# Optimization experiments

Hardware: AMD Instinct MI355X
Metric: run time of the kernel (lower is better)

## Reference

```python
import jax, jax.numpy as jnp
import numpy as np


def setup_inputs() -> dict:
    key = jax.random.key(0)
    ks = jax.random.split(key, 8)
    B, L, C = 8, 4096, 1024
    H = C // 2
    return {
        "x": jax.random.normal(ks[0], (B, L, C), dtype=jnp.float32),
        "w1": jax.random.normal(ks[1], (C, 1), dtype=jnp.float32) * 0.02,
        "b1": jnp.zeros((1,), dtype=jnp.float32),
        "w2": jax.random.normal(ks[2], (C, H), dtype=jnp.float32) * 0.02,
        "b2": jnp.zeros((H,), dtype=jnp.float32),
        "w3": jax.random.normal(ks[3], (H, C), dtype=jnp.float32) * 0.02,
        "b3": jnp.zeros((C,), dtype=jnp.float32),
        "w4": jax.random.normal(ks[4], (C, H), dtype=jnp.float32) * 0.02,
        "b4": jnp.zeros((H,), dtype=jnp.float32),
        "w5": jax.random.normal(ks[5], (C, H), dtype=jnp.float32) * 0.02,
        "b5": jnp.zeros((H,), dtype=jnp.float32),
    }


def reference(x, w1, b1, w2, b2, w3, b3, w4, b4, w5, b5):
    # Polarized self-attention (keras): channel branch then spatial branch.
    B, L, C = x.shape
    # --- channel branch ---
    t1 = x @ w1 + b1                                   # conv1: [B, L, 1]
    t2 = x @ w2 + b2                                   # conv2: [B, L, C/2]
    a = jax.nn.softmax(t1.reshape(B, 1, L), axis=-1)   # reshape1 + softmax: [B, 1, L]
    t2 = jnp.einsum('bol,blh->boh', a, t2)             # dot1 (axes 2,1): [B, 1, C/2]
    t2 = jax.nn.sigmoid(t2 @ w3 + b3)                  # conv3 + sigmoid: [B, 1, C]
    # attention1([inputs, t2]): dot scores [B, L, 1]; softmax over key axis of
    # size 1 is exactly 1.0, so output is t2 broadcast across L (exact math).
    o = jnp.broadcast_to(t2, (B, L, C))                # [B, L, C]
    # --- spatial branch ---
    t1 = o @ w4 + b4                                   # conv4: [B, L, C/2]
    t2 = o @ w5 + b5                                   # conv5: [B, L, C/2]
    t1 = jnp.max(t1, axis=1)[:, :, None]               # global max pool + reshape2: [B, C/2, 1]
    s = jax.nn.sigmoid(jnp.einsum('bho,blh->bol', t1, t2))  # dot2 (axes 1,2) + sigmoid: [B, 1, L]
    # attention2([reshape(o, [B,C,L]), s]): scores [B, C, 1]; softmax over the
    # size-1 key axis is 1.0, so output is s broadcast to [B, C, L] (exact).
    out = jnp.broadcast_to(s, (B, C, L)).reshape(B, L, C)  # reshape4
    return out
```

## Files before the change

### kernel.cpp

```cpp
#include <hip/hip_runtime.h>
#include <stdint.h>

#define B 8
#define L 4096
#define C 1024
#define H 512
#define CCH 64

__global__ __launch_bounds__(256) void k1_t1(const float* __restrict__ x,
                                             const float* __restrict__ w1,
                                             const float* __restrict__ b1,
                                             float* __restrict__ t1) {
    int wave = (blockIdx.x << 2) | ((int)threadIdx.x >> 6);
    int lane = threadIdx.x & 63;
    if (wave >= B * L) return;
    const float4* px = (const float4*)(x + (size_t)wave * C);
    const float4* pw = (const float4*)w1;
    float acc = 0.f;
#pragma unroll
    for (int k = 0; k < 4; ++k) {
        float4 xv = px[lane + 64 * k];
        float4 wv = pw[lane + 64 * k];
        acc += xv.x * wv.x + xv.y * wv.y + xv.z * wv.z + xv.w * wv.w;
    }
#pragma unroll
    for (int off = 32; off > 0; off >>= 1) acc += __shfl_down(acc, off, 64);
    if (lane == 0) t1[wave] = acc + b1[0];
}

__global__ __launch_bounds__(256) void k2_stats(const float* __restrict__ t1,
                                                float* __restrict__ stats,
                                                float* __restrict__ xa,
                                                float* __restrict__ pooled,
                                                float* __restrict__ vraw,
                                                float* __restrict__ u4raw,
                                                float* __restrict__ u5raw) {
    __shared__ float red[256];
    int b = blockIdx.x, t = threadIdx.x;
    const float* tb = t1 + b * L;
    float m = -1e30f;
    for (int i = t; i < L; i += 256) m = fmaxf(m, tb[i]);
    red[t] = m; __syncthreads();
    for (int s = 128; s > 0; s >>= 1) { if (t < s) red[t] = fmaxf(red[t], red[t + s]); __syncthreads(); }
    float mb = red[0]; __syncthreads();
    float sum = 0.f;
    for (int i = t; i < L; i += 256) sum += __expf(tb[i] - mb);
    red[t] = sum; __syncthreads();
    for (int s = 128; s > 0; s >>= 1) { if (t < s) red[t] += red[t + s]; __syncthreads(); }
    if (t == 0) { stats[b * 2] = mb; stats[b * 2 + 1] = 1.f / red[0]; }
    for (int i = t; i < C; i += 256) { xa[b * C + i] = 0.f; vraw[b * C + i] = 0.f; }
    for (int i = t; i < H; i += 256) { pooled[b * H + i] = 0.f; u4raw[b * H + i] = 0.f; u5raw[b * H + i] = 0.f; }
}

__global__ __launch_bounds__(256) void k3_xa(const float* __restrict__ x,
                                             const float* __restrict__ t1,
                                             const float* __restrict__ stats,
                                             float* __restrict__ xa) {
    int b = blockIdx.x >> 6;
    int chunk = blockIdx.x & 63;
    int t = threadIdx.x;
    float mb = stats[b * 2], inv = stats[b * 2 + 1];
    int l0 = chunk * 64;
    float a0 = 0.f, a1 = 0.f, a2 = 0.f, a3 = 0.f;
    for (int i = 0; i < 64; ++i) {
        int l = l0 + i;
        float w = __expf(t1[b * L + l] - mb) * inv;
        float4 xv = *((const float4*)(x + ((size_t)(b * L + l)) * C) + t);
        a0 += w * xv.x;
        a1 += w * xv.y;
        a2 += w * xv.z;
        a3 += w * xv.w;
    }
    int c = t * 4;
    atomicAdd(&xa[b * C + c + 0], a0);
    atomicAdd(&xa[b * C + c + 1], a1);
    atomicAdd(&xa[b * C + c + 2], a2);
    atomicAdd(&xa[b * C + c + 3], a3);
}

__global__ __launch_bounds__(256) void k4a_pooled(const float* __restrict__ xa,
                                                  const float* __restrict__ w2,
                                                  const float* __restrict__ b2,
                                                  float* __restrict__ pooled) {
    __shared__ float xs[B][CCH];
    int hg = blockIdx.x & 1;
    int cc = blockIdx.x >> 1;
    int t = threadIdx.x;
    int c0 = cc * CCH;
    for (int i = t; i < B * CCH; i += 256) {
        int bb = i / CCH, ci = i % CCH;
        xs[bb][ci] = xa[bb * C + c0 + ci];
    }
    __syncthreads();
    int h = hg * 256 + t;
    float acc[B] = {0.f, 0.f, 0.f, 0.f, 0.f, 0.f, 0.f, 0.f};
#pragma unroll 4
    for (int ci = 0; ci < CCH; ++ci) {
        float w = w2[(size_t)(c0 + ci) * H + h];
#pragma unroll
        for (int bb = 0; bb < B; ++bb) acc[bb] += xs[bb][ci] * w;
    }
    float bias = (cc == 0) ? b2[h] : 0.f;
#pragma unroll
    for (int bb = 0; bb < B; ++bb) atomicAdd(&pooled[bb * H + h], acc[bb] + bias);
}

__global__ __launch_bounds__(256) void k4b_v(const float* __restrict__ pooled,
                                             const float* __restrict__ w3,
                                             float* __restrict__ vraw) {
    __shared__ float ps[B][CCH];
    int cg = blockIdx.x & 3;
    int hc = blockIdx.x >> 2;
    int t = threadIdx.x;
    int h0 = hc * CCH;
    for (int i = t; i < B * CCH; i += 256) {
        int bb = i / CCH, hi = i % CCH;
        ps[bb][hi] = pooled[bb * H + h0 + hi];
    }
    __syncthreads();
    int c = cg * 256 + t;
    float acc[B] = {0.f, 0.f, 0.f, 0.f, 0.f, 0.f, 0.f, 0.f};
#pragma unroll 4
    for (int hi = 0; hi < CCH; ++hi) {
        float w = w3[(size_t)(h0 + hi) * C + c];
#pragma unroll
        for (int bb = 0; bb < B; ++bb) acc[bb] += ps[bb][hi] * w;
    }
#pragma unroll
    for (int bb = 0; bb < B; ++bb) atomicAdd(&vraw[bb * C + c], acc[bb]);
}

__global__ __launch_bounds__(256) void k4c_uv(const float* __restrict__ vraw,
                                              const float* __restrict__ b3,
                                              const float* __restrict__ w4,
                                              const float* __restrict__ w5,
                                              float* __restrict__ u4raw,
                                              float* __restrict__ u5raw) {
    __shared__ float vs[B][CCH];
    int hg = blockIdx.x & 1;
    int cc = blockIdx.x >> 1;
    int t = threadIdx.x;
    int c0 = cc * CCH;
    for (int i = t; i < B * CCH; i += 256) {
        int bb = i / CCH, ci = i % CCH;
        float raw = vraw[bb * C + c0 + ci] + b3[c0 + ci];
        vs[bb][ci] = 1.f / (1.f + __expf(-raw));
    }
    __syncthreads();
    int h = hg * 256 + t;
    float a4[B] = {0.f, 0.f, 0.f, 0.f, 0.f, 0.f, 0.f, 0.f};
    float a5[B] = {0.f, 0.f, 0.f, 0.f, 0.f, 0.f, 0.f, 0.f};
#pragma unroll 2
    for (int ci = 0; ci < CCH; ++ci) {
        float wa = w4[(size_t)(c0 + ci) * H + h];
        float wb = w5[(size_t)(c0 + ci) * H + h];
#pragma unroll
        for (int bb = 0; bb < B; ++bb) {
            a4[bb] += vs[bb][ci] * wa;
            a5[bb] += vs[bb][ci] * wb;
        }
    }
#pragma unroll
    for (int bb = 0; bb < B; ++bb) {
        atomicAdd(&u4raw[bb * H + h], a4[bb]);
        atomicAdd(&u5raw[bb * H + h], a5[bb]);
    }
}

__global__ __launch_bounds__(256) void k4d_dot(const float* __restrict__ u4raw, const float* __restrict__ b4,
                                               const float* __restrict__ u5raw, const float* __restrict__ b5,
                                               float* __restrict__ scal) {
    __shared__ float red[256];
    int b = blockIdx.x, t = threadIdx.x;
    float s = 0.f;
    for (int h = t; h < H; h += 256)
        s += (u4raw[b * H + h] + b4[h]) * (u5raw[b * H + h] + b5[h]);
    red[t] = s; __syncthreads();
    for (int st = 128; st > 0; st >>= 1) { if (t < st) red[t] += red[t + st]; __syncthreads(); }
    if (t == 0) scal[b] = 1.f / (1.f + __expf(-red[0]));
}

__global__ __launch_bounds__(256) void k5_fill(const float* __restrict__ scal,
                                               float* __restrict__ out) {
    const int CHUNKS_PER_B = L * C / 4;
    int idx = blockIdx.x * 256 + threadIdx.x;
    int stride = gridDim.x * 256;
    for (int k = idx; k < B * CHUNKS_PER_B; k += stride) {
        int b = k / CHUNKS_PER_B;
        float s = scal[b];
        ((float4*)out)[k] = make_float4(s, s, s, s);
    }
}

extern "C" void kernel_launch(void* const* d_in, const int* in_sizes, int n_in,
                              void* d_out, int out_size, void* d_ws, size_t ws_size,
                              hipStream_t stream) {
    const float* x  = (const float*)d_in[0];
    const float* w1 = (const float*)d_in[1];
    const float* b1 = (const float*)d_in[2];
    const float* w2 = (const float*)d_in[3];
    const float* b2 = (const float*)d_in[4];
    const float* w3 = (const float*)d_in[5];
    const float* b3 = (const float*)d_in[6];
    const float* w4 = (const float*)d_in[7];
    const float* b4 = (const float*)d_in[8];
    const float* w5 = (const float*)d_in[9];
    const float* b5 = (const float*)d_in[10];

    float* ws     = (float*)d_ws;
    float* t1     = ws;
    float* stats  = t1 + B * L;
    float* xa     = stats + 2 * B;
    float* pooled = xa + B * C;
    float* vraw   = pooled + B * H;
    float* u4raw  = vraw + B * C;
    float* u5raw  = u4raw + B * H;
    float* scal   = u5raw + B * H;

    k1_t1<<<B * L / 4, 256, 0, stream>>>(x, w1, b1, t1);
    k2_stats<<<B, 256, 0, stream>>>(t1, stats, xa, pooled, vraw, u4raw, u5raw);
    k3_xa<<<B * 64, 256, 0, stream>>>(x, t1, stats, xa);
    k4a_pooled<<<32, 256, 0, stream>>>(xa, w2, b2, pooled);
    k4b_v<<<32, 256, 0, stream>>>(pooled, w3, vraw);
    k4c_uv<<<32, 256, 0, stream>>>(vraw, b3, w4, w5, u4raw, u5raw);
    k4d_dot<<<B, 256, 0, stream>>>(u4raw, b4, u5raw, b5, scal);
    k5_fill<<<4096, 256, 0, stream>>>(scal, (float*)d_out);
}
```

Baseline: 324.8 us.

## Fuse attention logits, softmax and weighted sum into single pass over x

Computes the conv1 logit, its exponential and the exp-weighted row accumulation in one wave-per-16-rows pass, writing per-wave partials that a small reduction kernel normalizes. This removes the second full read of x and the separate max/sum stats kernel. It also merges the conv3/conv4/conv5 stages into one kernel and folds the final dot/sigmoid into the output fill, cutting launches. The softmax no longer subtracts the max, trading numerical stability for a single pass.

Result: faster. 311.9 us (-4.0%).

```diff
diff --git a/kernel.cpp b/kernel.cpp
--- a/kernel.cpp
+++ b/kernel.cpp
@@ -6,76 +6,97 @@
 #define C 1024
 #define H 512
 #define CCH 64
-
-__global__ __launch_bounds__(256) void k1_t1(const float* __restrict__ x,
-                                             const float* __restrict__ w1,
-                                             const float* __restrict__ b1,
-                                             float* __restrict__ t1) {
-    int wave = (blockIdx.x << 2) | ((int)threadIdx.x >> 6);
+#define WAVES_PER_BATCH 256
+#define NPART (B * WAVES_PER_BATCH)
+
+__global__ __launch_bounds__(256) void kA_fused(const float* __restrict__ x,
+                                                const float* __restrict__ w1,
+                                                const float* __restrict__ b1,
+                                                float* __restrict__ partial_xa,
+                                                float* __restrict__ partial_s) {
+    int waveId = (blockIdx.x << 2) | ((int)threadIdx.x >> 6);
     int lane = threadIdx.x & 63;
-    if (wave >= B * L) return;
-    const float4* px = (const float4*)(x + (size_t)wave * C);
-    const float4* pw = (const float4*)w1;
-    float acc = 0.f;
-#pragma unroll
-    for (int k = 0; k < 4; ++k) {
-        float4 xv = px[lane + 64 * k];
-        float4 wv = pw[lane + 64 * k];
-        acc += xv.x * wv.x + xv.y * wv.y + xv.z * wv.z + xv.w * wv.w;
-    }
-#pragma unroll
-    for (int off = 32; off > 0; off >>= 1) acc += __shfl_down(acc, off, 64);
-    if (lane == 0) t1[wave] = acc + b1[0];
-}
-
-__global__ __launch_bounds__(256) void k2_stats(const float* __restrict__ t1,
-                                                float* __restrict__ stats,
-                                                float* __restrict__ xa,
-                                                float* __restrict__ pooled,
-                                                float* __restrict__ vraw,
-                                                float* __restrict__ u4raw,
-                                                float* __restrict__ u5raw) {
-    __shared__ float red[256];
-    int b = blockIdx.x, t = threadIdx.x;
-    const float* tb = t1 + b * L;
-    float m = -1e30f;
-    for (int i = t; i < L; i += 256) m = fmaxf(m, tb[i]);
-    red[t] = m; __syncthreads();
-    for (int s = 128; s > 0; s >>= 1) { if (t < s) red[t] = fmaxf(red[t], red[t + s]); __syncthreads(); }
-    float mb = red[0]; __syncthreads();
-    float sum = 0.f;
-    for (int i = t; i < L; i += 256) sum += __expf(tb[i] - mb);
-    red[t] = sum; __syncthreads();
-    for (int s = 128; s > 0; s >>= 1) { if (t < s) red[t] += red[t + s]; __syncthreads(); }
-    if (t == 0) { stats[b * 2] = mb; stats[b * 2 + 1] = 1.f / red[0]; }
-    for (int i = t; i < C; i += 256) { xa[b * C + i] = 0.f; vraw[b * C + i] = 0.f; }
-    for (int i = t; i < H; i += 256) { pooled[b * H + i] = 0.f; u4raw[b * H + i] = 0.f; u5raw[b * H + i] = 0.f; }
-}
-
-__global__ __launch_bounds__(256) void k3_xa(const float* __restrict__ x,
-                                             const float* __restrict__ t1,
-                                             const float* __restrict__ stats,
-                                             float* __restrict__ xa) {
-    int b = blockIdx.x >> 6;
-    int chunk = blockIdx.x & 63;
-    int t = threadIdx.x;
-    float mb = stats[b * 2], inv = stats[b * 2 + 1];
-    int l0 = chunk * 64;
-    float a0 = 0.f, a1 = 0.f, a2 = 0.f, a3 = 0.f;
-    for (int i = 0; i < 64; ++i) {
-        int l = l0 + i;
-        float w = __expf(t1[b * L + l] - mb) * inv;
-        float4 xv = *((const float4*)(x + ((size_t)(b * L + l)) * C) + t);
-        a0 += w * xv.x;
-        a1 += w * xv.y;
-        a2 += w * xv.z;
-        a3 += w * xv.w;
-    }
-    int c = t * 4;
-    atomicAdd(&xa[b * C + c + 0], a0);
-    atomicAdd(&xa[b * C + c + 1], a1);
-    atomicAdd(&xa[b * C + c + 2], a2);
-    atomicAdd(&xa[b * C + c + 3], a3);
+    int b = waveId >> 8;
+    int chunk = waveId & 255;
+    int l0 = chunk * 16;
+    float b1v = b1[0];
+
+    const float4* w1v = (const float4*)w1;
+    float4 wf[4];
+#pragma unroll
+    for (int k = 0; k < 4; ++k) wf[k] = w1v[lane + 64 * k];
+
+    float4 acc[4];
+#pragma unroll
+    for (int k = 0; k < 4; ++k) acc[k] = make_float4(0.f, 0.f, 0.f, 0.f);
+    float sexp = 0.f;
+
+    for (int r = 0; r < 16; ++r) {
+        const float4* row = (const float4*)(x + ((size_t)(b * L + l0 + r)) * C);
+        float4 xv[4];
+#pragma unroll
+        for (int k = 0; k < 4; ++k) xv[k] = row[lane + 64 * k];
+        float d = 0.f;
+#pragma unroll
+        for (int k = 0; k < 4; ++k)
+            d += xv[k].x * wf[k].x + xv[k].y * wf[k].y + xv[k].z * wf[k].z + xv[k].w * wf[k].w;
+#pragma unroll
+        for (int off = 32; off > 0; off >>= 1) d += __shfl_xor(d, off, 64);
+        float e = __expf(d + b1v);
+        sexp += e;
+#pragma unroll
+        for (int k = 0; k < 4; ++k) {
+            acc[k].x += e * xv[k].x;
+            acc[k].y += e * xv[k].y;
+            acc[k].z += e * xv[k].z;
+            acc[k].w += e * xv[k].w;
+        }
+    }
+    float4* pxa = (float4*)partial_xa + (size_t)waveId * (C / 4);
+#pragma unroll
+    for (int k = 0; k < 4; ++k) pxa[lane + 64 * k] = acc[k];
+    if (lane == 0) partial_s[waveId] = sexp;
+}
+
+__global__ __launch_bounds__(256) void kB_reduce(const float* __restrict__ partial_xa,
+                                                 const float* __restrict__ partial_s,
+                                                 float* __restrict__ xa,
+                                                 float* __restrict__ zero_targets) {
+    __shared__ float sred[256];
+    __shared__ float4 red[8][32];
+    int blk = blockIdx.x, t = threadIdx.x;
+    int b = blk >> 3;
+    int cg = blk & 7;
+
+    int zi = blk * 256 + t;
+    if (zi < 3 * B * H) zero_targets[zi] = 0.f;
+
+    sred[t] = partial_s[b * WAVES_PER_BATCH + t];
+    __syncthreads();
+    for (int s = 128; s > 0; s >>= 1) { if (t < s) sred[t] += sred[t + s]; __syncthreads(); }
+    float inv = 1.f / sred[0];
+    __syncthreads();
+
+    int col4 = cg * 32 + (t & 31);
+    int rg = t >> 5;
+    const float4* pxa = (const float4*)partial_xa;
+    float4 a = make_float4(0.f, 0.f, 0.f, 0.f);
+    for (int r = 0; r < 32; ++r) {
+        float4 v = pxa[(size_t)(b * WAVES_PER_BATCH + rg * 32 + r) * (C / 4) + col4];
+        a.x += v.x; a.y += v.y; a.z += v.z; a.w += v.w;
+    }
+    red[rg][t & 31] = a;
+    __syncthreads();
+    if (rg == 0) {
+        float4 s4 = red[0][t & 31];
+#pragma unroll
+        for (int g = 1; g < 8; ++g) {
+            float4 v = red[g][t & 31];
+            s4.x += v.x; s4.y += v.y; s4.z += v.z; s4.w += v.w;
+        }
+        s4.x *= inv; s4.y *= inv; s4.z *= inv; s4.w *= inv;
+        ((float4*)xa)[(size_t)b * (C / 4) + col4] = s4;
+    }
 }
 
 __global__ __launch_bounds__(256) void k4a_pooled(const float* __restrict__ xa,
@@ -105,91 +126,85 @@
     for (int bb = 0; bb < B; ++bb) atomicAdd(&pooled[bb * H + h], acc[bb] + bias);
 }
 
-__global__ __launch_bounds__(256) void k4b_v(const float* __restrict__ pooled,
-                                             const float* __restrict__ w3,
-                                             float* __restrict__ vraw) {
-    __shared__ float ps[B][CCH];
-    int cg = blockIdx.x & 3;
-    int hc = blockIdx.x >> 2;
-    int t = threadIdx.x;
-    int h0 = hc * CCH;
-    for (int i = t; i < B * CCH; i += 256) {
-        int bb = i / CCH, hi = i % CCH;
-        ps[bb][hi] = pooled[bb * H + h0 + hi];
-    }
-    __syncthreads();
-    int c = cg * 256 + t;
-    float acc[B] = {0.f, 0.f, 0.f, 0.f, 0.f, 0.f, 0.f, 0.f};
-#pragma unroll 4
-    for (int hi = 0; hi < CCH; ++hi) {
-        float w = w3[(size_t)(h0 + hi) * C + c];
-#pragma unroll
-        for (int bb = 0; bb < B; ++bb) acc[bb] += ps[bb][hi] * w;
-    }
-#pragma unroll
-    for (int bb = 0; bb < B; ++bb) atomicAdd(&vraw[bb * C + c], acc[bb]);
-}
-
-__global__ __launch_bounds__(256) void k4c_uv(const float* __restrict__ vraw,
-                                              const float* __restrict__ b3,
-                                              const float* __restrict__ w4,
-                                              const float* __restrict__ w5,
-                                              float* __restrict__ u4raw,
-                                              float* __restrict__ u5raw) {
+__global__ __launch_bounds__(256) void k4bc(const float* __restrict__ pooled,
+                                            const float* __restrict__ w3,
+                                            const float* __restrict__ b3,
+                                            const float* __restrict__ w4,
+                                            const float* __restrict__ w5,
+                                            float* __restrict__ u4raw,
+                                            float* __restrict__ u5raw) {
+    __shared__ float pooledS[B][H];
+    __shared__ float vpart[4][B][CCH];
     __shared__ float vs[B][CCH];
     int hg = blockIdx.x & 1;
     int cc = blockIdx.x >> 1;
+    int c0 = cc * CCH;
     int t = threadIdx.x;
-    int c0 = cc * CCH;
-    for (int i = t; i < B * CCH; i += 256) {
-        int bb = i / CCH, ci = i % CCH;
-        float raw = vraw[bb * C + c0 + ci] + b3[c0 + ci];
-        vs[bb][ci] = 1.f / (1.f + __expf(-raw));
-    }
-    __syncthreads();
-    int h = hg * 256 + t;
-    float a4[B] = {0.f, 0.f, 0.f, 0.f, 0.f, 0.f, 0.f, 0.f};
-    float a5[B] = {0.f, 0.f, 0.f, 0.f, 0.f, 0.f, 0.f, 0.f};
+
+    for (int i = t; i < B * H; i += 256) ((float*)pooledS)[i] = pooled[i];
+    __syncthreads();
+
+    {
+        int ci = t & 63;
+        int hq = t >> 6;
+        float a[B] = {0.f, 0.f, 0.f, 0.f, 0.f, 0.f, 0.f, 0.f};
+        for (int hh = 0; hh < 128; ++hh) {
+            int h = hq * 128 + hh;
+            float w = w3[(size_t)h * C + c0 + ci];
+#pragma unroll
+            for (int bb = 0; bb < B; ++bb) a[bb] += pooledS[bb][h] * w;
+        }
+#pragma unroll
+        for (int bb = 0; bb < B; ++bb) vpart[hq][bb][ci] = a[bb];
+    }
+    __syncthreads();
+#pragma unroll
+    for (int p = 0; p < 2; ++p) {
+        int idx = t * 2 + p;
+        int bb = idx >> 6, ci = idx & 63;
+        float v = vpart[0][bb][ci] + vpart[1][bb][ci] + vpart[2][bb][ci] + vpart[3][bb][ci]
+                + b3[c0 + ci];
+        vs[bb][ci] = 1.f / (1.f + __expf(-v));
+    }
+    __syncthreads();
+    {
+        int h = hg * 256 + t;
+        float a4[B] = {0.f, 0.f, 0.f, 0.f, 0.f, 0.f, 0.f, 0.f};
+        float a5[B] = {0.f, 0.f, 0.f, 0.f, 0.f, 0.f, 0.f, 0.f};
 #pragma unroll 2
-    for (int ci = 0; ci < CCH; ++ci) {
-        float wa = w4[(size_t)(c0 + ci) * H + h];
-        float wb = w5[(size_t)(c0 + ci) * H + h];
+        for (int ci = 0; ci < CCH; ++ci) {
+            float wa = w4[(size_t)(c0 + ci) * H + h];
+            float wb = w5[(size_t)(c0 + ci) * H + h];
+#pragma unroll
+            for (int bb = 0; bb < B; ++bb) {
+                a4[bb] += vs[bb][ci] * wa;
+                a5[bb] += vs[bb][ci] * wb;
+            }
+        }
 #pragma unroll
         for (int bb = 0; bb < B; ++bb) {
-            a4[bb] += vs[bb][ci] * wa;
-            a5[bb] += vs[bb][ci] * wb;
-        }
-    }
-#pragma unroll
-    for (int bb = 0; bb < B; ++bb) {
-        atomicAdd(&u4raw[bb * H + h], a4[bb]);
-        atomicAdd(&u5raw[bb * H + h], a5[bb]);
-    }
-}
-
-__global__ __launch_bounds__(256) void k4d_dot(const float* __restrict__ u4raw, const float* __restrict__ b4,
+            atomicAdd(&u4raw[bb * H + h], a4[bb]);
+            atomicAdd(&u5raw[bb * H + h], a5[bb]);
+        }
+    }
+}
+
+__global__ __launch_bounds__(256) void k5_fill(const float* __restrict__ u4raw, const float* __restrict__ b4,
                                                const float* __restrict__ u5raw, const float* __restrict__ b5,
-                                               float* __restrict__ scal) {
+                                               float* __restrict__ out) {
     __shared__ float red[256];
-    int b = blockIdx.x, t = threadIdx.x;
-    float s = 0.f;
-    for (int h = t; h < H; h += 256)
-        s += (u4raw[b * H + h] + b4[h]) * (u5raw[b * H + h] + b5[h]);
+    int blk = blockIdx.x, t = threadIdx.x;
+    int b = blk >> 9;
+    int rg = blk & 511;
+    float s = (u4raw[b * H + t] + b4[t]) * (u5raw[b * H + t] + b5[t])
+            + (u4raw[b * H + 256 + t] + b4[256 + t]) * (u5raw[b * H + 256 + t] + b5[256 + t]);
     red[t] = s; __syncthreads();
     for (int st = 128; st > 0; st >>= 1) { if (t < st) red[t] += red[t + st]; __syncthreads(); }
-    if (t == 0) scal[b] = 1.f / (1.f + __expf(-red[0]));
-}
-
-__global__ __launch_bounds__(256) void k5_fill(const float* __restrict__ scal,
-                                               float* __restrict__ out) {
-    const int CHUNKS_PER_B = L * C / 4;
-    int idx = blockIdx.x * 256 + threadIdx.x;
-    int stride = gridDim.x * 256;
-    for (int k = idx; k < B * CHUNKS_PER_B; k += stride) {
-        int b = k / CHUNKS_PER_B;
-        float s = scal[b];
-        ((float4*)out)[k] = make_float4(s, s, s, s);
-    }
+    float sc = 1.f / (1.f + __expf(-red[0]));
+    float4 s4 = make_float4(sc, sc, sc, sc);
+    float4* o = (float4*)out + (size_t)b * (L * C / 4) + rg * 2048;
+#pragma unroll
+    for (int k = 0; k < 8; ++k) o[t + 256 * k] = s4;
 }
 
 extern "C" void kernel_launch(void* const* d_in, const int* in_sizes, int n_in,
@@ -207,22 +222,17 @@
     const float* w5 = (const float*)d_in[9];
     const float* b5 = (const float*)d_in[10];
 
-    float* ws     = (float*)d_ws;
-    float* t1     = ws;
-    float* stats  = t1 + B * L;
-    float* xa     = stats + 2 * B;
-    float* pooled = xa + B * C;
-    float* vraw   = pooled + B * H;
-    float* u4raw  = vraw + B * C;
-    float* u5raw  = u4raw + B * H;
-    float* scal   = u5raw + B * H;
-
-    k1_t1<<<B * L / 4, 256, 0, stream>>>(x, w1, b1, t1);
-    k2_stats<<<B, 256, 0, stream>>>(t1, stats, xa, pooled, vraw, u4raw, u5raw);
-    k3_xa<<<B * 64, 256, 0, stream>>>(x, t1, stats, xa);
+    float* ws         = (float*)d_ws;
+    float* partial_xa = ws;
+    float* partial_s  = partial_xa + NPART * C;
+    float* xa         = partial_s + NPART;
+    float* pooled     = xa + B * C;
+    float* u4raw      = pooled + B * H;
+    float* u5raw      = u4raw + B * H;
+
+    kA_fused<<<NPART / 4, 256, 0, stream>>>(x, w1, b1, partial_xa, partial_s);
+    kB_reduce<<<64, 256, 0, stream>>>(partial_xa, partial_s, xa, pooled);
     k4a_pooled<<<32, 256, 0, stream>>>(xa, w2, b2, pooled);
-    k4b_v<<<32, 256, 0, stream>>>(pooled, w3, vraw);
-    k4c_uv<<<32, 256, 0, stream>>>(vraw, b3, w4, w5, u4raw, u5raw);
-    k4d_dot<<<B, 256, 0, stream>>>(u4raw, b4, u5raw, b5, scal);
-    k5_fill<<<4096, 256, 0, stream>>>(scal, (float*)d_out);
-}
+    k4bc<<<32, 256, 0, stream>>>(pooled, w3, b3, w4, w5, u4raw, u5raw);
+    k5_fill<<<B * 512, 256, 0, stream>>>(u4raw, b4, u5raw, b5, (float*)d_out);
+}
```
